# Kernel tuning notes

Measured on AMD Instinct MI355X. Metric: run time of the kernel, lower is better.

Reference implementation:

```python
import jax, jax.numpy as jnp
import numpy as np
import math

B, S, D, H, HD, M, E = 4, 1024, 1024, 16, 64, 4096, 1024
EPS = 1e-6

def rms_norm(x, w):
    # torch: x / (||x||/sqrt(d) + eps) * w  (eps added to the norm, not norm^2)
    n = jnp.sqrt(jnp.sum(x * x, axis=-1, keepdims=True)) / math.sqrt(x.shape[-1])
    return x / (n + EPS) * w

def rope(x):
    # x: (B,H,S,hd)
    hd, s = x.shape[-1], x.shape[2]
    inv = 1.0 / (10000.0 ** (jnp.arange(0, hd, 2, dtype=jnp.float32) / hd))
    fr = jnp.arange(s, dtype=jnp.float32)[:, None] * inv[None, :]        # (S, hd/2)
    emb = jnp.concatenate([fr, fr], axis=-1)                              # (S, hd)
    cos, sin = jnp.cos(emb), jnp.sin(emb)
    x1, x2 = x[..., : hd // 2], x[..., hd // 2 :]
    rot = jnp.concatenate([-x2, x1], axis=-1)
    return x * cos + rot * sin

def setup_inputs() -> dict:
    key = jax.random.key(0)
    ks = jax.random.split(key, 18)
    p = lambda k, sh: jax.random.normal(k, sh, jnp.float32) * 0.02
    return {
        'x': jax.random.normal(ks[0], (B, S, D), jnp.float32),
        'emb': jax.random.normal(ks[1], (B, E), jnp.float32),
        'ln1_w': jnp.ones((D,), jnp.float32),
        'ln1_lW': p(ks[2], (E, 2 * D)), 'ln1_lb': p(ks[3], (2 * D,)),
        'ln2_w': jnp.ones((D,), jnp.float32),
        'ln2_lW': p(ks[4], (E, 2 * D)), 'ln2_lb': p(ks[5], (2 * D,)),
        'qkv_W': p(ks[6], (D, 3 * D)), 'qkv_b': p(ks[7], (3 * D,)),
        'proj_W': p(ks[8], (D, D)), 'proj_b': p(ks[9], (D,)),
        'nq_w': jnp.ones((HD,), jnp.float32), 'nk_w': jnp.ones((HD,), jnp.float32),
        'mlp_W': p(ks[10], (D, 2 * M)), 'mlp_b': p(ks[11], (2 * M,)),
        'out_W': p(ks[12], (M, D)), 'out_b': p(ks[13], (D,)),
        'gates_W': p(ks[14], (E, 2 * D)), 'gates_b': p(ks[15], (2 * D,)),
    }

def reference(x, emb, ln1_w, ln1_lW, ln1_lb, ln2_w, ln2_lW, ln2_lb,
              qkv_W, qkv_b, proj_W, proj_b, nq_w, nk_w,
              mlp_W, mlp_b, out_W, out_b, gates_W, gates_b):
    g = emb @ gates_W + gates_b                       # (B, 2D)
    gate_mha, gate_mlp = g[:, :D], g[:, D:]
    # AdaLNZero 1
    ss = emb @ ln1_lW + ln1_lb                        # (B, 2D): [scale | shift]
    xn = rms_norm(x, ln1_w) * (1.0 + ss[:, None, :D]) + ss[:, None, D:]
    # RoPE attention with qk RMSNorm
    qkv = (xn @ qkv_W + qkv_b).reshape(B, S, 3, H, HD).transpose(2, 0, 3, 1, 4)
    q, k, v = qkv[0], qkv[1], qkv[2]                  # each (B,H,S,HD)
    q = rms_norm(rope(q), nq_w)
    k = rms_norm(rope(k), nk_w)
    scores = jnp.einsum('bhqd,bhkd->bhqk', q, k) * (HD ** -0.5)
    attn = jnp.nan_to_num(jax.nn.softmax(scores, axis=-1))
    ao = jnp.einsum('bhqk,bhkd->bhqd', attn, v).transpose(0, 2, 1, 3).reshape(B, S, D)
    x = x + gate_mha[:, None, :] * (ao @ proj_W + proj_b)
    # AdaLNZero 2 + SwiGLU MLP
    ss2 = emb @ ln2_lW + ln2_lb
    xn2 = rms_norm(x, ln2_w) * (1.0 + ss2[:, None, :D]) + ss2[:, None, D:]
    h = xn2 @ mlp_W + mlp_b                           # (B,S,2M)
    act = h[..., :M] * jax.nn.silu(h[..., M:])
    mlp_out = act @ out_W + out_b
    return x + gate_mlp[:, None, :] * mlp_out
```

## Files before the change

### kernel.cpp

```cpp
#include <hip/hip_runtime.h>
#include <hip/hip_bf16.h>
#include <math.h>

#define B_ 4
#define S_ 1024
#define D_ 1024
#define H_ 16
#define HD_ 64
#define M_ 4096
#define E_ 1024

using bf16 = __hip_bfloat16;
typedef short bf16x8 __attribute__((ext_vector_type(8)));
typedef float f32x4 __attribute__((ext_vector_type(4)));

__device__ __forceinline__ void gl_lds16(const void* g, void* l) {
    __builtin_amdgcn_global_load_lds(
        (__attribute__((address_space(1))) void*)(g),
        (__attribute__((address_space(3))) void*)(l), 16, 0, 0);
}


__global__ __launch_bounds__(256) void transpose_kernel(
    const float* __restrict__ W, bf16* __restrict__ Wt, int K, int N)
{
    __shared__ float tile[32][33];
    int n0 = blockIdx.x * 32, k0 = blockIdx.y * 32;
    int tx = threadIdx.x & 31, ty = threadIdx.x >> 5;
    #pragma unroll
    for (int r = ty; r < 32; r += 8)
        tile[r][tx] = W[(long)(k0 + r) * N + n0 + tx];
    __syncthreads();
    #pragma unroll
    for (int r = ty; r < 32; r += 8)
        Wt[(long)(n0 + r) * K + k0 + tx] = __float2bfloat16(tile[tx][r]);
}

__global__ __launch_bounds__(256) void embgemm_kernel(
    const float* __restrict__ emb,
    const float* __restrict__ W0, const float* __restrict__ b0,
    const float* __restrict__ W1, const float* __restrict__ b1,
    const float* __restrict__ W2, const float* __restrict__ b2,
    float* __restrict__ G, float* __restrict__ SS, float* __restrict__ SS2)
{
    __shared__ float se[256];
    int b = blockIdx.y;
    int k0 = blockIdx.z * 256;
    if (threadIdx.x < 256) se[threadIdx.x] = emb[b * 1024 + k0 + threadIdx.x];
    __syncthreads();
    int j = blockIdx.x * 256 + threadIdx.x;
    int which = j >> 11, col = j & 2047;
    const float* W  = which == 0 ? W0 : (which == 1 ? W1 : W2);
    const float* bb = which == 0 ? b0 : (which == 1 ? b1 : b2);
    float acc = (k0 == 0) ? bb[col] : 0.f;
    #pragma unroll 4
    for (int k = 0; k < 256; ++k) acc += se[k] * W[(long)(k0 + k) * 2048 + col];
    float* out = which == 0 ? G : (which == 1 ? SS : SS2);
    atomicAdd(&out[b * 2048 + col], acc);
}

__global__ __launch_bounds__(256) void rmsmod_kernel(
    const float* __restrict__ x, const float* __restrict__ w,
    const float* __restrict__ ss, bf16* __restrict__ out)
{
    int row = blockIdx.x;
    int b = row >> 10;
    const float* xr = x + (long)row * D_;
    float4 v = ((const float4*)xr)[threadIdx.x];
    float ssum = v.x * v.x + v.y * v.y + v.z * v.z + v.w * v.w;
    #pragma unroll
    for (int off = 32; off; off >>= 1) ssum += __shfl_xor(ssum, off);
    __shared__ float red[4];
    if ((threadIdx.x & 63) == 0) red[threadIdx.x >> 6] = ssum;
    __syncthreads();
    float tot = red[0] + red[1] + red[2] + red[3];
    float n = sqrtf(tot) * (1.f / 32.f);
    float inv = 1.f / (n + 1e-6f);
    int d0 = threadIdx.x * 4;
    const float* ssb = ss + b * 2048;
    bf16 t[4];
    t[0] = __float2bfloat16(v.x * inv * w[d0 + 0] * (1.f + ssb[d0 + 0]) + ssb[D_ + d0 + 0]);
    t[1] = __float2bfloat16(v.y * inv * w[d0 + 1] * (1.f + ssb[d0 + 1]) + ssb[D_ + d0 + 1]);
    t[2] = __float2bfloat16(v.z * inv * w[d0 + 2] * (1.f + ssb[d0 + 2]) + ssb[D_ + d0 + 2]);
    t[3] = __float2bfloat16(v.w * inv * w[d0 + 3] * (1.f + ssb[d0 + 3]) + ssb[D_ + d0 + 3]);
    *(uint2*)&out[(long)row * D_ + d0] = *(uint2*)t;
}

__global__ __launch_bounds__(256) void gemm_kernel(
    const bf16* __restrict__ A, const bf16* __restrict__ Bt,
    const float* __restrict__ bias,
    bf16* __restrict__ Cb, float* __restrict__ Cf,
    const float* __restrict__ resid, const float* __restrict__ gates, int gate_off,
    int Mrows, int N, int K, int mode)
{
    __shared__ bf16 sA[128 * 32];
    __shared__ bf16 sB[128 * 32];
    const int tid = threadIdx.x;
    const int wave = tid >> 6, lane = tid & 63;
    const int num_pid_n = N >> 7;
    const int pid = blockIdx.x;
    const int group_size = 8 * num_pid_n;
    const int group_id = pid / group_size;
    const int pid_in = pid - group_id * group_size;
    const int pid_m = group_id * 8 + (pid_in & 7);
    const int pid_n = pid_in >> 3;
    const int m0 = pid_m * 128, n0 = pid_n * 128;
    const int wm = (wave & 1) * 64, wn = (wave >> 1) * 64;
    const int cl = lane & 15, qd = lane >> 4;

    f32x4 acc[4][4] = {};

    const int c0 = wave * 128 + lane, c1 = c0 + 64;
    const int r0 = c0 >> 2, s0 = (c0 & 3) ^ ((c0 >> 3) & 3);
    const int r1 = c1 >> 2, s1 = (c1 & 3) ^ ((c1 >> 3) & 3);
    const bf16* gA0 = A + (long)(m0 + r0) * K + s0 * 8;
    const bf16* gA1 = A + (long)(m0 + r1) * K + s1 * 8;
    const bf16* gB0 = Bt + (long)(n0 + r0) * K + s0 * 8;
    const bf16* gB1 = Bt + (long)(n0 + r1) * K + s1 * 8;
    bf16* lA0 = &sA[wave * 1024];
    bf16* lA1 = &sA[wave * 1024 + 512];
    bf16* lB0 = &sB[wave * 1024];
    bf16* lB1 = &sB[wave * 1024 + 512];

    const int q8s = (qd ^ ((cl >> 1) & 3)) * 8;

    for (int kc = 0; kc < K; kc += 32) {
        gl_lds16(gA0 + kc, lA0);
        gl_lds16(gA1 + kc, lA1);
        gl_lds16(gB0 + kc, lB0);
        gl_lds16(gB1 + kc, lB1);
        __syncthreads();
        bf16x8 af[4], bfr[4];
        #pragma unroll
        for (int t = 0; t < 4; ++t)
            af[t] = *(const bf16x8*)&sA[(wm + cl + t * 16) * 32 + q8s];
        #pragma unroll
        for (int u = 0; u < 4; ++u)
            bfr[u] = *(const bf16x8*)&sB[(wn + cl + u * 16) * 32 + q8s];
        #pragma unroll
        for (int t = 0; t < 4; ++t)
            #pragma unroll
            for (int u = 0; u < 4; ++u)
                acc[t][u] = __builtin_amdgcn_mfma_f32_16x16x32_bf16(af[t], bfr[u], acc[t][u], 0, 0, 0);
        __syncthreads();
    }

    #pragma unroll
    for (int t = 0; t < 4; ++t) {
        #pragma unroll
        for (int u = 0; u < 4; ++u) {
            int col = n0 + wn + u * 16 + cl;
            float bs = bias[col];
            #pragma unroll
            for (int i = 0; i < 4; ++i) {
                int row = m0 + wm + t * 16 + qd * 4 + i;
                float v = acc[t][u][i] + bs;
                if (mode == 0) {
                    Cb[(long)row * N + col] = __float2bfloat16(v);
                } else {
                    int b = row >> 10;
                    float g = gates[b * 2048 + gate_off + col];
                    Cf[(long)row * N + col] = resid[(long)row * N + col] + g * v;
                }
            }
        }
    }
}

__global__ __launch_bounds__(256) void gemm64_kernel(
    const bf16* __restrict__ A, const bf16* __restrict__ Bt,
    const float* __restrict__ bias,
    bf16* __restrict__ Cb, float* __restrict__ Cf,
    const float* __restrict__ resid, const float* __restrict__ gates, int gate_off,
    int Mrows, int N, int K, int mode)
{
    __shared__ bf16 sA[64 * 32];
    __shared__ bf16 sB[64 * 32];
    const int tid = threadIdx.x;
    const int wave = tid >> 6, lane = tid & 63;
    const int num_pid_n = N >> 6;
    const int pid = blockIdx.x;
    const int group_size = 8 * num_pid_n;
    const int group_id = pid / group_size;
    const int pid_in = pid - group_id * group_size;
    const int pid_m = group_id * 8 + (pid_in & 7);
    const int pid_n = pid_in >> 3;
    const int m0 = pid_m * 64, n0 = pid_n * 64;
    const int wm = (wave & 1) * 32, wn = (wave >> 1) * 32;
    const int cl = lane & 15, qd = lane >> 4;

    f32x4 acc[2][2] = {};

    const int c = tid;
    const int rr = c >> 2, ss = (c & 3) ^ ((c >> 3) & 3);
    const bf16* gA = A + (long)(m0 + rr) * K + ss * 8;
    const bf16* gB = Bt + (long)(n0 + rr) * K + ss * 8;
    bf16* lA = &sA[wave * 512];
    bf16* lB = &sB[wave * 512];

    const int q8s = (qd ^ ((cl >> 1) & 3)) * 8;

    for (int kc = 0; kc < K; kc += 32) {
        gl_lds16(gA + kc, lA);
        gl_lds16(gB + kc, lB);
        __syncthreads();
        bf16x8 af[2], bfr[2];
        #pragma unroll
        for (int t = 0; t < 2; ++t)
            af[t] = *(const bf16x8*)&sA[(wm + cl + t * 16) * 32 + q8s];
        #pragma unroll
        for (int u = 0; u < 2; ++u)
            bfr[u] = *(const bf16x8*)&sB[(wn + cl + u * 16) * 32 + q8s];
        #pragma unroll
        for (int t = 0; t < 2; ++t)
            #pragma unroll
            for (int u = 0; u < 2; ++u)
                acc[t][u] = __builtin_amdgcn_mfma_f32_16x16x32_bf16(af[t], bfr[u], acc[t][u], 0, 0, 0);
        __syncthreads();
    }

    #pragma unroll
    for (int t = 0; t < 2; ++t) {
        #pragma unroll
        for (int u = 0; u < 2; ++u) {
            int col = n0 + wn + u * 16 + cl;
            float bs = bias[col];
            #pragma unroll
            for (int i = 0; i < 4; ++i) {
                int row = m0 + wm + t * 16 + qd * 4 + i;
                float v = acc[t][u][i] + bs;
                if (mode == 0) {
                    Cb[(long)row * N + col] = __float2bfloat16(v);
                } else {
                    int b = row >> 10;
                    float g = gates[b * 2048 + gate_off + col];
                    Cf[(long)row * N + col] = resid[(long)row * N + col] + g * v;
                }
            }
        }
    }
}

__global__ __launch_bounds__(256) void gemm_mlp_kernel(
    const bf16* __restrict__ A, const bf16* __restrict__ Bt,
    const float* __restrict__ bias, bf16* __restrict__ ACT)
{
    __shared__ bf16 sA[128 * 32];
    __shared__ bf16 sB1[64 * 32];
    __shared__ bf16 sB2[64 * 32];
    const int tid = threadIdx.x;
    const int wave = tid >> 6, lane = tid & 63;
    const int num_pid_n = 64;
    const int pid = blockIdx.x;
    const int group_size = 8 * num_pid_n;
    const int group_id = pid / group_size;
    const int pid_in = pid - group_id * group_size;
    const int pid_m = group_id * 8 + (pid_in & 7);
    const int pid_n = pid_in >> 3;
    const int m0 = pid_m * 128, n0 = pid_n * 64;
    const int wm = (wave & 1) * 64, wn = (wave >> 1) * 32;
    const int cl = lane & 15, qd = lane >> 4;
    const int K = 1024;

    f32x4 acc1[4][2] = {};
    f32x4 acc2[4][2] = {};

    const int c0 = wave * 128 + lane, c1 = c0 + 64;
    const int ra0 = c0 >> 2, sa0 = (c0 & 3) ^ ((c0 >> 3) & 3);
    const int ra1 = c1 >> 2, sa1 = (c1 & 3) ^ ((c1 >> 3) & 3);
    const int rb = tid >> 2, sb = (tid & 3) ^ ((tid >> 3) & 3);
    const bf16* gA0 = A + (long)(m0 + ra0) * K + sa0 * 8;
    const bf16* gA1 = A + (long)(m0 + ra1) * K + sa1 * 8;
    const bf16* gB1 = Bt + (long)(n0 + rb) * K + sb * 8;
    const bf16* gB2 = Bt + (long)(4096 + n0 + rb) * K + sb * 8;
    bf16* lA0 = &sA[wave * 1024];
    bf16* lA1 = &sA[wave * 1024 + 512];
    bf16* lB1 = &sB1[wave * 512];
    bf16* lB2 = &sB2[wave * 512];

    const int q8s = (qd ^ ((cl >> 1) & 3)) * 8;

    for (int kc = 0; kc < K; kc += 32) {
        gl_lds16(gA0 + kc, lA0);
        gl_lds16(gA1 + kc, lA1);
        gl_lds16(gB1 + kc, lB1);
        gl_lds16(gB2 + kc, lB2);
        __syncthreads();
        bf16x8 af[4], b1[2], b2[2];
        #pragma unroll
        for (int t = 0; t < 4; ++t)
            af[t] = *(const bf16x8*)&sA[(wm + cl + t * 16) * 32 + q8s];
        #pragma unroll
        for (int u = 0; u < 2; ++u) {
            b1[u] = *(const bf16x8*)&sB1[(wn + cl + u * 16) * 32 + q8s];
            b2[u] = *(const bf16x8*)&sB2[(wn + cl + u * 16) * 32 + q8s];
        }
        #pragma unroll
        for (int t = 0; t < 4; ++t)
            #pragma unroll
            for (int u = 0; u < 2; ++u) {
                acc1[t][u] = __builtin_amdgcn_mfma_f32_16x16x32_bf16(af[t], b1[u], acc1[t][u], 0, 0, 0);
                acc2[t][u] = __builtin_amdgcn_mfma_f32_16x16x32_bf16(af[t], b2[u], acc2[t][u], 0, 0, 0);
            }
        __syncthreads();
    }

    #pragma unroll
    for (int t = 0; t < 4; ++t) {
        #pragma unroll
        for (int u = 0; u < 2; ++u) {
            int col = n0 + wn + u * 16 + cl;
            float bs1 = bias[col];
            float bs2 = bias[4096 + col];
            #pragma unroll
            for (int i = 0; i < 4; ++i) {
                int row = m0 + wm + t * 16 + qd * 4 + i;
                float h1 = acc1[t][u][i] + bs1;
                float h2 = acc2[t][u][i] + bs2;
                float sg = 1.f / (1.f + __expf(-h2));
                ACT[(long)row * 4096 + col] = __float2bfloat16(h1 * h2 * sg);
            }
        }
    }
}

__global__ __launch_bounds__(256) void ropenorm_kernel(
    const bf16* __restrict__ qkv, const float* __restrict__ nq_w, const float* __restrict__ nk_w,
    bf16* __restrict__ qh, bf16* __restrict__ kh, bf16* __restrict__ vt)
{
    int gid = blockIdx.x * 4 + (threadIdx.x >> 6);
    int lane = threadIdx.x & 63;
    int b = gid >> 14, s = (gid >> 4) & (S_ - 1), h = gid & (H_ - 1);
    const long base = (long)(b * S_ + s) * 3072 + h * 64 + lane;
    float qv = __bfloat162float(qkv[base]);
    float kv = __bfloat162float(qkv[base + 1024]);
    float vv = __bfloat162float(qkv[base + 2048]);
    int j = lane & 31;
    float inv = exp2f(-(float)j * (13.287712379549449f / 32.f));
    float ang = (float)s * inv;
    float sn, c;
    sincosf(ang, &sn, &c);
    float pq = __shfl_xor(qv, 32);
    float pk = __shfl_xor(kv, 32);
    float rq = (lane < 32) ? -pq : pq;
    float rk = (lane < 32) ? -pk : pk;
    float qr = qv * c + rq * sn;
    float kr = kv * c + rk * sn;
    float sq = qr * qr, sk = kr * kr;
    #pragma unroll
    for (int off = 32; off; off >>= 1) { sq += __shfl_xor(sq, off); sk += __shfl_xor(sk, off); }
    float nq = sqrtf(sq) * 0.125f;
    float nk = sqrtf(sk) * 0.125f;
    float qo = qr / (nq + 1e-6f) * nq_w[lane];
    float ko = kr / (nk + 1e-6f) * nk_w[lane];
    long hb = ((long)(b * H_ + h) * S_ + s) * 64 + lane;
    qh[hb] = __float2bfloat16(qo);
    kh[hb] = __float2bfloat16(ko);
    vt[((long)(b * H_ + h) * 64 + lane) * S_ + s] = __float2bfloat16(vv);
}

__global__ __launch_bounds__(256) void attn_kernel(
    const bf16* __restrict__ qh, const bf16* __restrict__ kh, const bf16* __restrict__ vt,
    bf16* __restrict__ ao)
{
    const int bh = blockIdx.y;
    const int q0 = blockIdx.x * 64;
    const int tid = threadIdx.x, wave = tid >> 6, lane = tid & 63;
    const int cl = lane & 15, qd = lane >> 4;

    __shared__ bf16 sQ[64 * 72];
    __shared__ bf16 sK[64 * 72];
    __shared__ bf16 sV[64 * 72];
    __shared__ bf16 sP[4][16 * 72];

    {
        const bf16* Qg = qh + (long)bh * S_ * 64 + (long)q0 * 64;
        int a = tid, b2 = tid + 256;
        *(uint4*)&sQ[(a >> 3) * 72 + (a & 7) * 8]  = *(const uint4*)&Qg[(a >> 3) * 64 + (a & 7) * 8];
        *(uint4*)&sQ[(b2 >> 3) * 72 + (b2 & 7) * 8] = *(const uint4*)&Qg[(b2 >> 3) * 64 + (b2 & 7) * 8];
    }

    float l_i[4] = {0.f, 0.f, 0.f, 0.f};
    f32x4 o_acc[4] = {};

    const bf16* Kg = kh + (long)bh * S_ * 64;
    const bf16* Vg = vt + (long)bh * 64 * S_;

    for (int kv0 = 0; kv0 < S_; kv0 += 64) {
        __syncthreads();
        {
            int a = tid, b2 = tid + 256;
            *(uint4*)&sK[(a >> 3) * 72 + (a & 7) * 8]   = *(const uint4*)&Kg[((long)kv0 + (a >> 3)) * 64 + (a & 7) * 8];
            *(uint4*)&sK[(b2 >> 3) * 72 + (b2 & 7) * 8] = *(const uint4*)&Kg[((long)kv0 + (b2 >> 3)) * 64 + (b2 & 7) * 8];
            *(uint4*)&sV[(a >> 3) * 72 + (a & 7) * 8]   = *(const uint4*)&Vg[(long)(a >> 3) * S_ + kv0 + (a & 7) * 8];
            *(uint4*)&sV[(b2 >> 3) * 72 + (b2 & 7) * 8] = *(const uint4*)&Vg[(long)(b2 >> 3) * S_ + kv0 + (b2 & 7) * 8];
        }
        __syncthreads();

        f32x4 sfr[4] = {};
        #pragma unroll
        for (int u = 0; u < 4; ++u) {
            #pragma unroll
            for (int ks = 0; ks < 2; ++ks) {
                bf16x8 aq = *(const bf16x8*)&sQ[(wave * 16 + cl) * 72 + ks * 32 + qd * 8];
                bf16x8 bk = *(const bf16x8*)&sK[(u * 16 + cl) * 72 + ks * 32 + qd * 8];
                sfr[u] = __builtin_amdgcn_mfma_f32_16x16x32_bf16(aq, bk, sfr[u], 0, 0, 0);
            }
        }

        #pragma unroll
        for (int i = 0; i < 4; ++i) {
            float sum = 0.f;
            #pragma unroll
            for (int u = 0; u < 4; ++u) {
                float p = __expf(sfr[u][i] * 0.125f - 8.f);
                sum += p;
                sP[wave][(qd * 4 + i) * 72 + u * 16 + cl] = __float2bfloat16(p);
            }
            sum += __shfl_xor(sum, 1);
            sum += __shfl_xor(sum, 2);
            sum += __shfl_xor(sum, 4);
            sum += __shfl_xor(sum, 8);
            l_i[i] += sum;
        }

        #pragma unroll
        for (int ks = 0; ks < 2; ++ks) {
            bf16x8 ap = *(const bf16x8*)&sP[wave][cl * 72 + ks * 32 + qd * 8];
            #pragma unroll
            for (int u = 0; u < 4; ++u) {
                bf16x8 bv = *(const bf16x8*)&sV[(u * 16 + cl) * 72 + ks * 32 + qd * 8];
                o_acc[u] = __builtin_amdgcn_mfma_f32_16x16x32_bf16(ap, bv, o_acc[u], 0, 0, 0);
            }
        }
    }

    #pragma unroll
    for (int i = 0; i < 4; ++i) {
        float invl = 1.f / l_i[i];
        int row = q0 + wave * 16 + qd * 4 + i;
        #pragma unroll
        for (int u = 0; u < 4; ++u) {
            int d = u * 16 + cl;
            ao[((long)(bh >> 4) * S_ + row) * D_ + (bh & 15) * 64 + d] =
                __float2bfloat16(o_acc[u][i] * invl);
        }
    }
}

extern "C" void kernel_launch(void* const* d_in, const int* in_sizes, int n_in,
                              void* d_out, int out_size, void* d_ws, size_t ws_size,
                              hipStream_t stream) {
    const float* x       = (const float*)d_in[0];
    const float* emb     = (const float*)d_in[1];
    const float* ln1_w   = (const float*)d_in[2];
    const float* ln1_lW  = (const float*)d_in[3];
    const float* ln1_lb  = (const float*)d_in[4];
    const float* ln2_w   = (const float*)d_in[5];
    const float* ln2_lW  = (const float*)d_in[6];
    const float* ln2_lb  = (const float*)d_in[7];
    const float* qkv_W   = (const float*)d_in[8];
    const float* qkv_b   = (const float*)d_in[9];
    const float* proj_W  = (const float*)d_in[10];
    const float* proj_b  = (const float*)d_in[11];
    const float* nq_w    = (const float*)d_in[12];
    const float* nk_w    = (const float*)d_in[13];
    const float* mlp_W   = (const float*)d_in[14];
    const float* mlp_b   = (const float*)d_in[15];
    const float* out_W   = (const float*)d_in[16];
    const float* out_b   = (const float*)d_in[17];
    const float* gates_W = (const float*)d_in[18];
    const float* gates_b = (const float*)d_in[19];
    float* out = (float*)d_out;

    char* p = (char*)d_ws;
    if (ws_size < 159481856UL) return;
    bf16* WT_QKV  = (bf16*)p;  p += 6291456;
    bf16* WT_PROJ = (bf16*)p;  p += 2097152;
    bf16* WT_MLP  = (bf16*)p;  p += 16777216;
    bf16* WT_OUT  = (bf16*)p;  p += 8388608;
    float* G      = (float*)p; p += 32768;
    float* SSb    = (float*)p; p += 32768;
    float* SS2b   = (float*)p; p += 32768;
    float* X1     = (float*)p; p += 16777216;
    bf16* XN2     = (bf16*)p;  p += 8388608;
    bf16* ACT     = (bf16*)p;  p += 33554432;
    char* REG = p;
    bf16* XN   = (bf16*)(REG);
    bf16* QKV  = (bf16*)(REG + 8388608);
    bf16* QH   = (bf16*)(REG + 33554432);
    bf16* KH   = (bf16*)(REG + 41943040);
    bf16* VT   = (bf16*)(REG + 50331648);
    bf16* AO   = (bf16*)(REG + 58720256);

    dim3 blk(256);
    hipMemsetAsync(G, 0, 98304, stream);
    transpose_kernel<<<dim3(96, 32),  blk, 0, stream>>>(qkv_W,  WT_QKV, 1024, 3072);
    transpose_kernel<<<dim3(32, 32),  blk, 0, stream>>>(proj_W, WT_PROJ, 1024, 1024);
    transpose_kernel<<<dim3(256, 32), blk, 0, stream>>>(mlp_W,  WT_MLP, 1024, 8192);
    transpose_kernel<<<dim3(32, 128), blk, 0, stream>>>(out_W,  WT_OUT, 4096, 1024);
    embgemm_kernel<<<dim3(24, 4, 4), blk, 0, stream>>>(emb, gates_W, gates_b, ln1_lW, ln1_lb,
                                                       ln2_lW, ln2_lb, G, SSb, SS2b);
    rmsmod_kernel<<<dim3(4096), blk, 0, stream>>>(x, ln1_w, SSb, XN);
    gemm_kernel<<<dim3(768), blk, 0, stream>>>(XN, WT_QKV, qkv_b, QKV, nullptr,
                                               nullptr, nullptr, 0, 4096, 3072, 1024, 0);
    ropenorm_kernel<<<dim3(16384), blk, 0, stream>>>(QKV, nq_w, nk_w, QH, KH, VT);
    attn_kernel<<<dim3(16, 64), blk, 0, stream>>>(QH, KH, VT, AO);
    gemm64_kernel<<<dim3(1024), blk, 0, stream>>>(AO, WT_PROJ, proj_b, nullptr, X1,
                                                  x, G, 0, 4096, 1024, 1024, 1);
    rmsmod_kernel<<<dim3(4096), blk, 0, stream>>>(X1, ln2_w, SS2b, XN2);
    gemm_mlp_kernel<<<dim3(2048), blk, 0, stream>>>(XN2, WT_MLP, mlp_b, ACT);
    gemm64_kernel<<<dim3(1024), blk, 0, stream>>>(ACT, WT_OUT, out_b, nullptr, out,
                                                  X1, G, 1024, 4096, 1024, 4096, 1);
}
```

Measured before the change: 513.6 us.

## Replace QKV and MLP GEMMs with 256x256 double-buffered pipelined 8-wave kernels

Swaps the 128-tile single-buffered GEMMs for the QKV projection and the fused SwiGLU MLP up-projection with a 256x256 tile, 512-thread kernel. It uses a double-buffered LDS ring with a K-step of 64, prefetches two tiles ahead, interleaves global-to-LDS copies between MFMA quadrants with barriers and setprio, and remaps blocks across XCDs. The goal is more data reuse per tile and latency hiding that the old one-tile-per-sync loop lacked. In exchange it uses 128KB of LDS and many more accumulator registers, and the grid becomes small (192 blocks for QKV), which may leave some CUs idle.

```diff
diff --git a/kernel.cpp b/kernel.cpp
--- a/kernel.cpp
+++ b/kernel.cpp
@@ -18,6 +18,11 @@
     __builtin_amdgcn_global_load_lds(
         (__attribute__((address_space(1))) void*)(g),
         (__attribute__((address_space(3))) void*)(l), 16, 0, 0);
+}
+
+__device__ __forceinline__ bf16x8 frag_ld(const char* base, int lbyte) {
+    int p = lbyte ^ (((lbyte >> 9) & 1) << 5);
+    return *(const bf16x8*)(base + p);
 }
 
 
@@ -86,82 +91,196 @@
     *(uint2*)&out[(long)row * D_ + d0] = *(uint2*)t;
 }
 
-__global__ __launch_bounds__(256) void gemm_kernel(
+
+#define STG_A(q, pb, kc) gl_lds16(A  + gAoff[q] + (kc), &sA[pb][(q) * 4096 + tid * 8])
+#define STG_B(q, pb, kc) gl_lds16(Bt + gBoff[q] + (kc), &sB[pb][(q) * 4096 + tid * 8])
+
+#define MFMA_QUAD(MH, NH, BF)                                                             \
+    __builtin_amdgcn_s_setprio(1);                                                        \
+    _Pragma("unroll")                                                                     \
+    for (int m = 0; m < 4; ++m) {                                                         \
+        _Pragma("unroll")                                                                 \
+        for (int n = 0; n < 2; ++n) {                                                     \
+            acc[(MH)*4+m][(NH)*2+n] = __builtin_amdgcn_mfma_f32_16x16x32_bf16(            \
+                aF[m][0], BF[n][0], acc[(MH)*4+m][(NH)*2+n], 0, 0, 0);                    \
+            acc[(MH)*4+m][(NH)*2+n] = __builtin_amdgcn_mfma_f32_16x16x32_bf16(            \
+                aF[m][1], BF[n][1], acc[(MH)*4+m][(NH)*2+n], 0, 0, 0);                    \
+        }                                                                                 \
+    }                                                                                     \
+    __builtin_amdgcn_s_setprio(0);
+
+#define GEMM256_LOOP                                                                      \
+    const int nt = K >> 6;                                                                \
+    for (int t = 0; t < nt; ++t) {                                                        \
+        const int pb = t & 1;                                                             \
+        const char* cA = (const char*)sA[pb];                                             \
+        const char* cB = (const char*)sB[pb];                                             \
+        const int kc2 = (t + 2) << 6;                                                     \
+        const bool pf = (t + 2) < nt;                                                     \
+        bf16x8 aF[4][2], b0F[2][2], b1F[2][2];                                            \
+                                          \
+        _Pragma("unroll")                                                                 \
+        for (int m = 0; m < 4; ++m) {                                                     \
+            aF[m][0] = frag_ld(cA, rbA + m * 2048);                                       \
+            aF[m][1] = frag_ld(cA, rbA + m * 2048 + 64);                                  \
+        }                                                                                 \
+        _Pragma("unroll")                                                                 \
+        for (int n = 0; n < 2; ++n) {                                                     \
+            b0F[n][0] = frag_ld(cB, rbB + n * 2048);                                      \
+            b0F[n][1] = frag_ld(cB, rbB + n * 2048 + 64);                                 \
+        }                                                                                 \
+        __builtin_amdgcn_s_barrier();                                                     \
+        MFMA_QUAD(0, 0, b0F)                                                              \
+        __builtin_amdgcn_s_barrier();                                                     \
+                         \
+        _Pragma("unroll")                                                                 \
+        for (int n = 0; n < 2; ++n) {                                                     \
+            b1F[n][0] = frag_ld(cB, rbB + 4096 + n * 2048);                               \
+            b1F[n][1] = frag_ld(cB, rbB + 4096 + n * 2048 + 64);                          \
+        }                                                                                 \
+        if (pf) { STG_A(0, pb, kc2); STG_A(2, pb, kc2); }                                 \
+        __builtin_amdgcn_s_barrier();                                                     \
+        MFMA_QUAD(0, 1, b1F)                                                              \
+        __builtin_amdgcn_s_barrier();                                                     \
+                               \
+        _Pragma("unroll")                                                                 \
+        for (int m = 0; m < 4; ++m) {                                                     \
+            aF[m][0] = frag_ld(cA, rbA + 8192 + m * 2048);                                \
+            aF[m][1] = frag_ld(cA, rbA + 8192 + m * 2048 + 64);                           \
+        }                                                                                 \
+        if (pf) { STG_B(0, pb, kc2); STG_B(1, pb, kc2);                                   \
+                  STG_B(2, pb, kc2); STG_B(3, pb, kc2); }                                 \
+        __builtin_amdgcn_s_barrier();                                                     \
+        MFMA_QUAD(1, 1, b1F)                                                              \
+        __builtin_amdgcn_s_barrier();                                                     \
+                                 \
+        if (pf) { STG_A(1, pb, kc2); STG_A(3, pb, kc2); }                                 \
+        __builtin_amdgcn_s_barrier();                                                     \
+        MFMA_QUAD(1, 0, b0F)                                                              \
+        if (pf)              { asm volatile("s_waitcnt vmcnt(8)" ::: "memory"); }         \
+        else if (t + 1 < nt) { asm volatile("s_waitcnt vmcnt(0)" ::: "memory"); }         \
+        __builtin_amdgcn_s_barrier();                                                     \
+    }
+
+__global__ __launch_bounds__(512) void gemm256_kernel(
     const bf16* __restrict__ A, const bf16* __restrict__ Bt,
-    const float* __restrict__ bias,
-    bf16* __restrict__ Cb, float* __restrict__ Cf,
-    const float* __restrict__ resid, const float* __restrict__ gates, int gate_off,
-    int Mrows, int N, int K, int mode)
-{
-    __shared__ bf16 sA[128 * 32];
-    __shared__ bf16 sB[128 * 32];
+    const float* __restrict__ bias, bf16* __restrict__ Cb,
+    int N, int K)
+{
+    __shared__ bf16 sA[2][16384];
+    __shared__ bf16 sB[2][16384];
     const int tid = threadIdx.x;
     const int wave = tid >> 6, lane = tid & 63;
-    const int num_pid_n = N >> 7;
-    const int pid = blockIdx.x;
+    const int wr = wave >> 2, wc = wave & 3;
+    const int cl = lane & 15, qd = lane >> 4;
+
+    const int num_pid_n = N >> 8;
+    const int cpx = gridDim.x >> 3;
+    int wg = (blockIdx.x & 7) * cpx + (blockIdx.x >> 3);
     const int group_size = 8 * num_pid_n;
-    const int group_id = pid / group_size;
-    const int pid_in = pid - group_id * group_size;
-    const int pid_m = group_id * 8 + (pid_in & 7);
-    const int pid_n = pid_in >> 3;
-    const int m0 = pid_m * 128, n0 = pid_n * 128;
-    const int wm = (wave & 1) * 64, wn = (wave >> 1) * 64;
+    const int group_id = wg / group_size;
+    const int pid_in = wg - group_id * group_size;
+    const int m0 = (group_id * 8 + (pid_in & 7)) * 256;
+    const int n0 = (pid_in >> 3) * 256;
+
+    long gAoff[4], gBoff[4];
+    #pragma unroll
+    for (int q = 0; q < 4; ++q) {
+        int c = tid + q * 512;
+        int cs = c ^ (((c >> 5) & 1) << 1);
+        int row = cs >> 3, col = (cs & 7) * 8;
+        gAoff[q] = (long)(m0 + row) * K + col;
+        gBoff[q] = (long)(n0 + row) * K + col;
+    }
+
+    #pragma unroll
+    for (int q = 0; q < 4; ++q) { STG_A(q, 0, 0); STG_B(q, 0, 0); }
+    #pragma unroll
+    for (int q = 0; q < 4; ++q) { STG_A(q, 1, 64); STG_B(q, 1, 64); }
+
+    f32x4 acc[8][4] = {};
+    const int rbA = (wr * 128 + cl) * 128 + qd * 16;
+    const int rbB = (wc * 64 + cl) * 128 + qd * 16;
+
+    asm volatile("s_waitcnt vmcnt(8)" ::: "memory");
+    __builtin_amdgcn_s_barrier();
+
+    GEMM256_LOOP
+
+    #pragma unroll
+    for (int m = 0; m < 8; ++m) {
+        #pragma unroll
+        for (int n = 0; n < 4; ++n) {
+            int col = n0 + wc * 64 + n * 16 + cl;
+            float bs = bias[col];
+            #pragma unroll
+            for (int i = 0; i < 4; ++i) {
+                int row = m0 + wr * 128 + m * 16 + qd * 4 + i;
+                Cb[(long)row * N + col] = __float2bfloat16(acc[m][n][i] + bs);
+            }
+        }
+    }
+}
+
+__global__ __launch_bounds__(512) void gemm256_mlp_kernel(
+    const bf16* __restrict__ A, const bf16* __restrict__ Bt,
+    const float* __restrict__ bias, bf16* __restrict__ ACT, int K)
+{
+    __shared__ bf16 sA[2][16384];
+    __shared__ bf16 sB[2][16384];
+    const int tid = threadIdx.x;
+    const int wave = tid >> 6, lane = tid & 63;
+    const int wr = wave >> 2, wc = wave & 3;
     const int cl = lane & 15, qd = lane >> 4;
 
-    f32x4 acc[4][4] = {};
-
-    const int c0 = wave * 128 + lane, c1 = c0 + 64;
-    const int r0 = c0 >> 2, s0 = (c0 & 3) ^ ((c0 >> 3) & 3);
-    const int r1 = c1 >> 2, s1 = (c1 & 3) ^ ((c1 >> 3) & 3);
-    const bf16* gA0 = A + (long)(m0 + r0) * K + s0 * 8;
-    const bf16* gA1 = A + (long)(m0 + r1) * K + s1 * 8;
-    const bf16* gB0 = Bt + (long)(n0 + r0) * K + s0 * 8;
-    const bf16* gB1 = Bt + (long)(n0 + r1) * K + s1 * 8;
-    bf16* lA0 = &sA[wave * 1024];
-    bf16* lA1 = &sA[wave * 1024 + 512];
-    bf16* lB0 = &sB[wave * 1024];
-    bf16* lB1 = &sB[wave * 1024 + 512];
-
-    const int q8s = (qd ^ ((cl >> 1) & 3)) * 8;
-
-    for (int kc = 0; kc < K; kc += 32) {
-        gl_lds16(gA0 + kc, lA0);
-        gl_lds16(gA1 + kc, lA1);
-        gl_lds16(gB0 + kc, lB0);
-        gl_lds16(gB1 + kc, lB1);
-        __syncthreads();
-        bf16x8 af[4], bfr[4];
-        #pragma unroll
-        for (int t = 0; t < 4; ++t)
-            af[t] = *(const bf16x8*)&sA[(wm + cl + t * 16) * 32 + q8s];
-        #pragma unroll
-        for (int u = 0; u < 4; ++u)
-            bfr[u] = *(const bf16x8*)&sB[(wn + cl + u * 16) * 32 + q8s];
-        #pragma unroll
-        for (int t = 0; t < 4; ++t)
-            #pragma unroll
-            for (int u = 0; u < 4; ++u)
-                acc[t][u] = __builtin_amdgcn_mfma_f32_16x16x32_bf16(af[t], bfr[u], acc[t][u], 0, 0, 0);
-        __syncthreads();
-    }
-
-    #pragma unroll
-    for (int t = 0; t < 4; ++t) {
-        #pragma unroll
-        for (int u = 0; u < 4; ++u) {
-            int col = n0 + wn + u * 16 + cl;
-            float bs = bias[col];
+    const int num_pid_n = 32;
+    const int cpx = gridDim.x >> 3;
+    int wg = (blockIdx.x & 7) * cpx + (blockIdx.x >> 3);
+    const int group_size = 8 * num_pid_n;
+    const int group_id = wg / group_size;
+    const int pid_in = wg - group_id * group_size;
+    const int m0 = (group_id * 8 + (pid_in & 7)) * 256;
+    const int n0 = (pid_in >> 3) * 128;
+
+    long gAoff[4], gBoff[4];
+    #pragma unroll
+    for (int q = 0; q < 4; ++q) {
+        int c = tid + q * 512;
+        int cs = c ^ (((c >> 5) & 1) << 1);
+        int row = cs >> 3, col = (cs & 7) * 8;
+        gAoff[q] = (long)(m0 + row) * K + col;
+        int pp = row >> 5, hf = (row >> 4) & 1, wi = row & 15;
+        gBoff[q] = (long)(hf * 4096 + n0 + pp * 16 + wi) * K + col;
+    }
+
+    #pragma unroll
+    for (int q = 0; q < 4; ++q) { STG_A(q, 0, 0); STG_B(q, 0, 0); }
+    #pragma unroll
+    for (int q = 0; q < 4; ++q) { STG_A(q, 1, 64); STG_B(q, 1, 64); }
+
+    f32x4 acc[8][4] = {};
+    const int rbA = (wr * 128 + cl) * 128 + qd * 16;
+    const int rbB = (wc * 64 + cl) * 128 + qd * 16;
+
+    asm volatile("s_waitcnt vmcnt(8)" ::: "memory");
+    __builtin_amdgcn_s_barrier();
+
+    GEMM256_LOOP
+
+    #pragma unroll
+    for (int m = 0; m < 8; ++m) {
+        #pragma unroll
+        for (int pr = 0; pr < 2; ++pr) {
+            int col = n0 + wc * 32 + pr * 16 + cl;
+            float bs1 = bias[col];
+            float bs2 = bias[4096 + col];
             #pragma unroll
             for (int i = 0; i < 4; ++i) {
-                int row = m0 + wm + t * 16 + qd * 4 + i;
-                float v = acc[t][u][i] + bs;
-                if (mode == 0) {
-                    Cb[(long)row * N + col] = __float2bfloat16(v);
-                } else {
-                    int b = row >> 10;
-                    float g = gates[b * 2048 + gate_off + col];
-                    Cf[(long)row * N + col] = resid[(long)row * N + col] + g * v;
-                }
+                int row = m0 + wr * 128 + m * 16 + qd * 4 + i;
+                float h1 = acc[m][pr * 2 + 0][i] + bs1;
+                float h2 = acc[m][pr * 2 + 1][i] + bs2;
+                float sg = 1.f / (1.f + __expf(-h2));
+                ACT[(long)row * 4096 + col] = __float2bfloat16(h1 * h2 * sg);
             }
         }
     }
@@ -236,89 +355,6 @@
                     float g = gates[b * 2048 + gate_off + col];
                     Cf[(long)row * N + col] = resid[(long)row * N + col] + g * v;
                 }
-            }
-        }
-    }
-}
-
-__global__ __launch_bounds__(256) void gemm_mlp_kernel(
-    const bf16* __restrict__ A, const bf16* __restrict__ Bt,
-    const float* __restrict__ bias, bf16* __restrict__ ACT)
-{
-    __shared__ bf16 sA[128 * 32];
-    __shared__ bf16 sB1[64 * 32];
-    __shared__ bf16 sB2[64 * 32];
-    const int tid = threadIdx.x;
-    const int wave = tid >> 6, lane = tid & 63;
-    const int num_pid_n = 64;
-    const int pid = blockIdx.x;
-    const int group_size = 8 * num_pid_n;
-    const int group_id = pid / group_size;
-    const int pid_in = pid - group_id * group_size;
-    const int pid_m = group_id * 8 + (pid_in & 7);
-    const int pid_n = pid_in >> 3;
-    const int m0 = pid_m * 128, n0 = pid_n * 64;
-    const int wm = (wave & 1) * 64, wn = (wave >> 1) * 32;
-    const int cl = lane & 15, qd = lane >> 4;
-    const int K = 1024;
-
-    f32x4 acc1[4][2] = {};
-    f32x4 acc2[4][2] = {};
-
-    const int c0 = wave * 128 + lane, c1 = c0 + 64;
-    const int ra0 = c0 >> 2, sa0 = (c0 & 3) ^ ((c0 >> 3) & 3);
-    const int ra1 = c1 >> 2, sa1 = (c1 & 3) ^ ((c1 >> 3) & 3);
-    const int rb = tid >> 2, sb = (tid & 3) ^ ((tid >> 3) & 3);
-    const bf16* gA0 = A + (long)(m0 + ra0) * K + sa0 * 8;
-    const bf16* gA1 = A + (long)(m0 + ra1) * K + sa1 * 8;
-    const bf16* gB1 = Bt + (long)(n0 + rb) * K + sb * 8;
-    const bf16* gB2 = Bt + (long)(4096 + n0 + rb) * K + sb * 8;
-    bf16* lA0 = &sA[wave * 1024];
-    bf16* lA1 = &sA[wave * 1024 + 512];
-    bf16* lB1 = &sB1[wave * 512];
-    bf16* lB2 = &sB2[wave * 512];
-
-    const int q8s = (qd ^ ((cl >> 1) & 3)) * 8;
-
-    for (int kc = 0; kc < K; kc += 32) {
-        gl_lds16(gA0 + kc, lA0);
-        gl_lds16(gA1 + kc, lA1);
-        gl_lds16(gB1 + kc, lB1);
-        gl_lds16(gB2 + kc, lB2);
-        __syncthreads();
-        bf16x8 af[4], b1[2], b2[2];
-        #pragma unroll
-        for (int t = 0; t < 4; ++t)
-            af[t] = *(const bf16x8*)&sA[(wm + cl + t * 16) * 32 + q8s];
-        #pragma unroll
-        for (int u = 0; u < 2; ++u) {
-            b1[u] = *(const bf16x8*)&sB1[(wn + cl + u * 16) * 32 + q8s];
-            b2[u] = *(const bf16x8*)&sB2[(wn + cl + u * 16) * 32 + q8s];
-        }
-        #pragma unroll
-        for (int t = 0; t < 4; ++t)
-            #pragma unroll
-            for (int u = 0; u < 2; ++u) {
-                acc1[t][u] = __builtin_amdgcn_mfma_f32_16x16x32_bf16(af[t], b1[u], acc1[t][u], 0, 0, 0);
-                acc2[t][u] = __builtin_amdgcn_mfma_f32_16x16x32_bf16(af[t], b2[u], acc2[t][u], 0, 0, 0);
-            }
-        __syncthreads();
-    }
-
-    #pragma unroll
-    for (int t = 0; t < 4; ++t) {
-        #pragma unroll
-        for (int u = 0; u < 2; ++u) {
-            int col = n0 + wn + u * 16 + cl;
-            float bs1 = bias[col];
-            float bs2 = bias[4096 + col];
-            #pragma unroll
-            for (int i = 0; i < 4; ++i) {
-                int row = m0 + wm + t * 16 + qd * 4 + i;
-                float h1 = acc1[t][u][i] + bs1;
-                float h2 = acc2[t][u][i] + bs2;
-                float sg = 1.f / (1.f + __expf(-h2));
-                ACT[(long)row * 4096 + col] = __float2bfloat16(h1 * h2 * sg);
             }
         }
     }
@@ -502,14 +538,13 @@
     embgemm_kernel<<<dim3(24, 4, 4), blk, 0, stream>>>(emb, gates_W, gates_b, ln1_lW, ln1_lb,
                                                        ln2_lW, ln2_lb, G, SSb, SS2b);
     rmsmod_kernel<<<dim3(4096), blk, 0, stream>>>(x, ln1_w, SSb, XN);
-    gemm_kernel<<<dim3(768), blk, 0, stream>>>(XN, WT_QKV, qkv_b, QKV, nullptr,
-                                               nullptr, nullptr, 0, 4096, 3072, 1024, 0);
+    gemm256_kernel<<<dim3(192), dim3(512), 0, stream>>>(XN, WT_QKV, qkv_b, QKV, 3072, 1024);
     ropenorm_kernel<<<dim3(16384), blk, 0, stream>>>(QKV, nq_w, nk_w, QH, KH, VT);
     attn_kernel<<<dim3(16, 64), blk, 0, stream>>>(QH, KH, VT, AO);
     gemm64_kernel<<<dim3(1024), blk, 0, stream>>>(AO, WT_PROJ, proj_b, nullptr, X1,
                                                   x, G, 0, 4096, 1024, 1024, 1);
     rmsmod_kernel<<<dim3(4096), blk, 0, stream>>>(X1, ln2_w, SS2b, XN2);
-    gemm_mlp_kernel<<<dim3(2048), blk, 0, stream>>>(XN2, WT_MLP, mlp_b, ACT);
+    gemm256_mlp_kernel<<<dim3(512), dim3(512), 0, stream>>>(XN2, WT_MLP, mlp_b, ACT, 1024);
     gemm64_kernel<<<dim3(1024), blk, 0, stream>>>(ACT, WT_OUT, out_b, nullptr, out,
                                                   X1, G, 1024, 4096, 1024, 4096, 1);
 }
```

Result: no change. 506.8 us (-1.3%).
